# Optimization experiments

Hardware: AMD Instinct MI355X
Metric: run time of the kernel (lower is better)

## Reference

```python
import jax, jax.numpy as jnp
import numpy as np

# TT-matrix embedding: vocab = 50*60*60 = 180000, embed_dim = 8*8*8 = 512, tt_rank = 16
M1, M2, M3 = 50, 60, 60        # row modes (index factorization)
N1, N2, N3 = 8, 8, 8           # col modes (embedding-dim factorization)
R = 16                         # TT rank
SENT, BATCH = 2048, 64
VOCAB = M1 * M2 * M3


def setup_inputs() -> dict:
    key = jax.random.key(0)
    k1, k2, k3, kx = jax.random.split(key, 4)
    scale = 0.3  # per-core stddev (t3.random_matrix uses a similar per-core normal init)
    # core k stored with the gathered (row-mode) axis first so gather is a plain take
    core1 = jax.random.normal(k1, (M1, N1, R), dtype=jnp.float32) * scale       # [m1, n1, r]
    core2 = jax.random.normal(k2, (M2, R, N2, R), dtype=jnp.float32) * scale    # [m2, r, n2, r]
    core3 = jax.random.normal(k3, (M3, R, N3), dtype=jnp.float32) * scale       # [m3, r, n3]
    x = jax.random.randint(kx, (SENT, BATCH), 0, VOCAB, dtype=jnp.int64)        # batch_dim_last=True layout
    return {"x": x, "core1": core1, "core2": core2, "core3": core3}


def reference(x, core1, core2, core3):
    # batch_dim_last=True: x is [sent, batch] -> permute to [batch, sent]
    sent, batch = x.shape
    flat = x.T.reshape(-1)                      # [T] flat token ids, T = batch*sent
    # t3.ind2sub: row-major mixed-radix decomposition over row modes [M1, M2, M3]
    i1 = flat // (M2 * M3)
    rem = flat % (M2 * M3)
    i2 = rem // M3
    i3 = rem % M3
    # gather one slice per TT core
    g1 = core1[i1]                              # [T, n1, r]
    g2 = core2[i2]                              # [T, r, n2, r]
    g3 = core3[i3]                              # [T, r, n3]
    # contract cores -> full embedding rows (t3.gather_rows(...).full())
    t12 = jnp.einsum('tar,trbs->tabs', g1, g2)  # [T, n1, n2, r]
    emb = jnp.einsum('tabs,tsc->tabc', t12, g3) # [T, n1, n2, n3]
    rows = emb.reshape(batch, sent, N1 * N2 * N3)
    # batch_dim_last=True: permute back to [sent, batch, emb_dim]
    return rows.transpose(1, 0, 2)
```

## Files before the change

### kernel.cpp

```cpp
#include <hip/hip_runtime.h>
#include <hip/hip_bf16.h>


#define M2M3 3600u
#define M3 60u

__global__ __launch_bounds__(256) void tt_pair_kernel(
    const float* __restrict__ c1,
    const float* __restrict__ c2,
    float* __restrict__ tab)
{
    const int pair = blockIdx.x;
    const int i1 = pair / 60;
    const int i2 = pair - i1 * 60;
    const int tid = threadIdx.x;
    const int q  = tid >> 6;
    const int ab = tid & 63;
    const int a  = ab >> 3;
    const int b  = ab & 7;

    const float* __restrict__ g1 = c1 + i1 * 128 + a * 16;
    const float* __restrict__ g2 = c2 + i2 * 2048 + b * 16 + q * 4;

    float4 acc = make_float4(0.f, 0.f, 0.f, 0.f);
#pragma unroll
    for (int r = 0; r < 16; ++r) {
        const float a1 = g1[r];
        const float4 v = *(const float4*)(g2 + r * 128);
        acc.x = fmaf(a1, v.x, acc.x);
        acc.y = fmaf(a1, v.y, acc.y);
        acc.z = fmaf(a1, v.z, acc.z);
        acc.w = fmaf(a1, v.w, acc.w);
    }
    *(float4*)(tab + (size_t)pair * 1024 + tid * 4) = acc;
}

__global__ __launch_bounds__(256) void tt_embed2_kernel(
    const int* __restrict__ x,
    const float* __restrict__ c3,
    const float* __restrict__ tab,
    float* __restrict__ out,
    int T)
{
    const int u    = (int)((blockIdx.x * blockDim.x + threadIdx.x) >> 6);
    const int lane = threadIdx.x & 63;
    if (u >= T) return;

    const unsigned id  = __builtin_amdgcn_readfirstlane((unsigned)x[u]);
    const unsigned i1  = id / M2M3;
    const unsigned rem = id - i1 * M2M3;
    const unsigned i2  = rem / M3;
    const unsigned i3  = rem - i2 * M3;

    const float* tp = tab + (size_t)(i1 * 60u + i2) * 1024u;
    float4 t[4];
#pragma unroll
    for (int q = 0; q < 4; ++q)
        t[q] = *(const float4*)(tp + q * 256 + lane * 4);
    const float* tf = (const float*)t;

    const float4* __restrict__ g3 = (const float4*)(c3 + i3 * 128u);

    float o[8];
#pragma unroll
    for (int c = 0; c < 8; ++c) o[c] = 0.f;

#pragma unroll
    for (int s = 0; s < 16; ++s) {
        const float ts = tf[s];
        const float4 w0 = g3[s * 2 + 0];
        const float4 w1 = g3[s * 2 + 1];
        o[0] = fmaf(ts, w0.x, o[0]);
        o[1] = fmaf(ts, w0.y, o[1]);
        o[2] = fmaf(ts, w0.z, o[2]);
        o[3] = fmaf(ts, w0.w, o[3]);
        o[4] = fmaf(ts, w1.x, o[4]);
        o[5] = fmaf(ts, w1.y, o[5]);
        o[6] = fmaf(ts, w1.z, o[6]);
        o[7] = fmaf(ts, w1.w, o[7]);
    }

    float4* dst = (float4*)(out + (size_t)u * 512 + lane * 8);
    dst[0] = make_float4(o[0], o[1], o[2], o[3]);
    dst[1] = make_float4(o[4], o[5], o[6], o[7]);
}

__global__ __launch_bounds__(256) void tt_embed_kernel(
    const int* __restrict__ x, const float* __restrict__ c1,
    const float* __restrict__ c2, const float* __restrict__ c3,
    float* __restrict__ out, int T)
{
    const int u    = (int)((blockIdx.x * blockDim.x + threadIdx.x) >> 6);
    const int lane = threadIdx.x & 63;
    if (u >= T) return;
    const int a = lane >> 3, b = lane & 7;
    const unsigned id  = (unsigned)x[u];
    const unsigned i1  = id / M2M3;
    const unsigned rem = id - i1 * M2M3;
    const unsigned i2  = rem / M3;
    const unsigned i3  = rem - i2 * M3;
    const float4* g1 = (const float4*)(c1 + i1 * 128u + a * 16);
    const float*  g2 = c2 + i2 * 2048u + b * 16;
    const float4* g3 = (const float4*)(c3 + i3 * 128u);
    float4 a1v[4];
#pragma unroll
    for (int q = 0; q < 4; ++q) a1v[q] = g1[q];
    const float* a1f = (const float*)a1v;
    float t12[16];
#pragma unroll
    for (int s = 0; s < 16; ++s) t12[s] = 0.f;
#pragma unroll
    for (int r = 0; r < 16; ++r) {
        const float a1 = a1f[r];
        const float4* row = (const float4*)(g2 + r * 128);
#pragma unroll
        for (int q = 0; q < 4; ++q) {
            const float4 v = row[q];
            t12[q*4+0] = fmaf(a1, v.x, t12[q*4+0]);
            t12[q*4+1] = fmaf(a1, v.y, t12[q*4+1]);
            t12[q*4+2] = fmaf(a1, v.z, t12[q*4+2]);
            t12[q*4+3] = fmaf(a1, v.w, t12[q*4+3]);
        }
    }
    float o[8];
#pragma unroll
    for (int c = 0; c < 8; ++c) o[c] = 0.f;
#pragma unroll
    for (int s = 0; s < 16; ++s) {
        const float ts = t12[s];
        const float4 w0 = g3[s*2+0];
        const float4 w1 = g3[s*2+1];
        o[0]=fmaf(ts,w0.x,o[0]); o[1]=fmaf(ts,w0.y,o[1]);
        o[2]=fmaf(ts,w0.z,o[2]); o[3]=fmaf(ts,w0.w,o[3]);
        o[4]=fmaf(ts,w1.x,o[4]); o[5]=fmaf(ts,w1.y,o[5]);
        o[6]=fmaf(ts,w1.z,o[6]); o[7]=fmaf(ts,w1.w,o[7]);
    }
    float4* dst = (float4*)(out + (size_t)u * 512 + lane * 8);
    dst[0] = make_float4(o[0], o[1], o[2], o[3]);
    dst[1] = make_float4(o[4], o[5], o[6], o[7]);
}

extern "C" void kernel_launch(void* const* d_in, const int* in_sizes, int n_in,
                              void* d_out, int out_size, void* d_ws, size_t ws_size,
                              hipStream_t stream) {
    const int*   x  = (const int*)d_in[0];
    const float* c1 = (const float*)d_in[1];
    const float* c2 = (const float*)d_in[2];
    const float* c3 = (const float*)d_in[3];
    float* out = (float*)d_out;

    const int T = in_sizes[0];
    const size_t tab_bytes = 3000u * 1024u * sizeof(float);

    if (ws_size >= tab_bytes) {
        float* tab = (float*)d_ws;
        tt_pair_kernel<<<3000, 256, 0, stream>>>(c1, c2, tab);
        const int blocks = (T + 3) / 4;
        tt_embed2_kernel<<<blocks, 256, 0, stream>>>(x, c3, tab, out, T);
    } else {
        const int blocks = (T + 3) / 4;
        tt_embed_kernel<<<blocks, 256, 0, stream>>>(x, c1, c2, c3, out, T);
    }
}
```

Measured before the change: 334.3 us.

## Counting-sort tokens by (i1,i2) pair to reuse precomputed table rows

Adds a counting sort of tokens by their (i1,i2) pair index (histogram, single-block scan, atomic scatter) so each wavefront handles a chunk of tokens sharing table rows and reloads the 4KB pair row only when the pair changes. This is meant to cut redundant gathers from the 12MB pair table. It adds four extra kernel launches, global atomics, and scattered output writes, since consecutive sorted tokens land at random output rows.

```diff
diff --git a/kernel.cpp b/kernel.cpp
--- a/kernel.cpp
+++ b/kernel.cpp
@@ -1,9 +1,10 @@
 #include <hip/hip_runtime.h>
-#include <hip/hip_bf16.h>
 
 
 #define M2M3 3600u
-#define M3 60u
+#define M3   60u
+#define NPAIR 3000
+#define CHUNK 16
 
 __global__ __launch_bounds__(256) void tt_pair_kernel(
     const float* __restrict__ c1,
@@ -35,51 +36,156 @@
     *(float4*)(tab + (size_t)pair * 1024 + tid * 4) = acc;
 }
 
-__global__ __launch_bounds__(256) void tt_embed2_kernel(
-    const int* __restrict__ x,
+__global__ __launch_bounds__(256) void tt_zero_counts(unsigned* __restrict__ counts)
+{
+    const int i = blockIdx.x * blockDim.x + threadIdx.x;
+    if (i < NPAIR) counts[i] = 0u;
+}
+
+__global__ __launch_bounds__(256) void tt_hist(
+    const int* __restrict__ x, unsigned* __restrict__ counts, int T)
+{
+    const int t = blockIdx.x * blockDim.x + threadIdx.x;
+    if (t >= T) return;
+    const unsigned id = (unsigned)x[t];
+    atomicAdd(&counts[id / M3], 1u);
+}
+
+__global__ __launch_bounds__(1024) void tt_scan(
+    const unsigned* __restrict__ counts, unsigned* __restrict__ cursor)
+{
+    __shared__ unsigned buf[1024];
+    const int tid = threadIdx.x;
+    const int b = tid * 3;
+    unsigned c0 = 0, c1 = 0, c2 = 0;
+    if (b     < NPAIR) c0 = counts[b];
+    if (b + 1 < NPAIR) c1 = counts[b + 1];
+    if (b + 2 < NPAIR) c2 = counts[b + 2];
+    const unsigned local = c0 + c1 + c2;
+    buf[tid] = local;
+    __syncthreads();
+    for (int off = 1; off < 1024; off <<= 1) {
+        const unsigned v = (tid >= off) ? buf[tid - off] : 0u;
+        __syncthreads();
+        buf[tid] += v;
+        __syncthreads();
+    }
+    const unsigned excl = buf[tid] - local;
+    if (b     < NPAIR) cursor[b]     = excl;
+    if (b + 1 < NPAIR) cursor[b + 1] = excl + c0;
+    if (b + 2 < NPAIR) cursor[b + 2] = excl + c0 + c1;
+}
+
+__global__ __launch_bounds__(256) void tt_scatter(
+    const int* __restrict__ x, unsigned* __restrict__ cursor,
+    unsigned* __restrict__ recT, unsigned* __restrict__ recPI, int T)
+{
+    const int t = blockIdx.x * blockDim.x + threadIdx.x;
+    if (t >= T) return;
+    const unsigned id   = (unsigned)x[t];
+    const unsigned pair = id / M3;
+    const unsigned i3   = id - pair * M3;
+    const unsigned pos  = atomicAdd(&cursor[pair], 1u);
+    recT[pos]  = (unsigned)t;
+    recPI[pos] = (pair << 6) | i3;
+}
+
+__global__ __launch_bounds__(256) void tt_embed_sorted(
+    const unsigned* __restrict__ recT,
+    const unsigned* __restrict__ recPI,
     const float* __restrict__ c3,
     const float* __restrict__ tab,
     float* __restrict__ out,
     int T)
 {
+    const int wid  = (int)((blockIdx.x * blockDim.x + threadIdx.x) >> 6);
+    const int lane = threadIdx.x & 63;
+    const int base = wid * CHUNK;
+    if (base >= T) return;
+
+    unsigned rT = 0u, rP = 0u;
+    if (lane < CHUNK && base + lane < T) {
+        rT = recT[base + lane];
+        rP = recPI[base + lane];
+    }
+
+    const int n = min(CHUNK, T - base);
+    float4 t4[4];
+    int cur = -1;
+
+    for (int j = 0; j < n; ++j) {
+        const unsigned tt = __builtin_amdgcn_readlane(rT, j);
+        const unsigned pi = __builtin_amdgcn_readlane(rP, j);
+        const int      pair = (int)(pi >> 6);
+        const unsigned i3   = pi & 63u;
+
+        if (pair != cur) {
+            cur = pair;
+            const float* tp = tab + (size_t)pair * 1024u;
+#pragma unroll
+            for (int q = 0; q < 4; ++q)
+                t4[q] = *(const float4*)(tp + q * 256 + lane * 4);
+        }
+        const float* tf = (const float*)t4;
+
+        const float4* __restrict__ g3 = (const float4*)(c3 + i3 * 128u);
+
+        float o[8];
+#pragma unroll
+        for (int c = 0; c < 8; ++c) o[c] = 0.f;
+#pragma unroll
+        for (int s = 0; s < 16; ++s) {
+            const float ts = tf[s];
+            const float4 w0 = g3[s * 2 + 0];
+            const float4 w1 = g3[s * 2 + 1];
+            o[0] = fmaf(ts, w0.x, o[0]);
+            o[1] = fmaf(ts, w0.y, o[1]);
+            o[2] = fmaf(ts, w0.z, o[2]);
+            o[3] = fmaf(ts, w0.w, o[3]);
+            o[4] = fmaf(ts, w1.x, o[4]);
+            o[5] = fmaf(ts, w1.y, o[5]);
+            o[6] = fmaf(ts, w1.z, o[6]);
+            o[7] = fmaf(ts, w1.w, o[7]);
+        }
+
+        float4* dst = (float4*)(out + (size_t)tt * 512u + lane * 8);
+        dst[0] = make_float4(o[0], o[1], o[2], o[3]);
+        dst[1] = make_float4(o[4], o[5], o[6], o[7]);
+    }
+}
+
+__global__ __launch_bounds__(256) void tt_embed2_kernel(
+    const int* __restrict__ x, const float* __restrict__ c3,
+    const float* __restrict__ tab, float* __restrict__ out, int T)
+{
     const int u    = (int)((blockIdx.x * blockDim.x + threadIdx.x) >> 6);
     const int lane = threadIdx.x & 63;
     if (u >= T) return;
-
     const unsigned id  = __builtin_amdgcn_readfirstlane((unsigned)x[u]);
     const unsigned i1  = id / M2M3;
     const unsigned rem = id - i1 * M2M3;
     const unsigned i2  = rem / M3;
     const unsigned i3  = rem - i2 * M3;
-
     const float* tp = tab + (size_t)(i1 * 60u + i2) * 1024u;
     float4 t[4];
 #pragma unroll
     for (int q = 0; q < 4; ++q)
         t[q] = *(const float4*)(tp + q * 256 + lane * 4);
     const float* tf = (const float*)t;
-
     const float4* __restrict__ g3 = (const float4*)(c3 + i3 * 128u);
-
     float o[8];
 #pragma unroll
     for (int c = 0; c < 8; ++c) o[c] = 0.f;
-
 #pragma unroll
     for (int s = 0; s < 16; ++s) {
         const float ts = tf[s];
         const float4 w0 = g3[s * 2 + 0];
         const float4 w1 = g3[s * 2 + 1];
-        o[0] = fmaf(ts, w0.x, o[0]);
-        o[1] = fmaf(ts, w0.y, o[1]);
-        o[2] = fmaf(ts, w0.z, o[2]);
-        o[3] = fmaf(ts, w0.w, o[3]);
-        o[4] = fmaf(ts, w1.x, o[4]);
-        o[5] = fmaf(ts, w1.y, o[5]);
-        o[6] = fmaf(ts, w1.z, o[6]);
-        o[7] = fmaf(ts, w1.w, o[7]);
-    }
-
+        o[0]=fmaf(ts,w0.x,o[0]); o[1]=fmaf(ts,w0.y,o[1]);
+        o[2]=fmaf(ts,w0.z,o[2]); o[3]=fmaf(ts,w0.w,o[3]);
+        o[4]=fmaf(ts,w1.x,o[4]); o[5]=fmaf(ts,w1.y,o[5]);
+        o[6]=fmaf(ts,w1.z,o[6]); o[7]=fmaf(ts,w1.w,o[7]);
+    }
     float4* dst = (float4*)(out + (size_t)u * 512 + lane * 8);
     dst[0] = make_float4(o[0], o[1], o[2], o[3]);
     dst[1] = make_float4(o[4], o[5], o[6], o[7]);
@@ -150,11 +256,34 @@
     float* out = (float*)d_out;
 
     const int T = in_sizes[0];
-    const size_t tab_bytes = 3000u * 1024u * sizeof(float);
-
-    if (ws_size >= tab_bytes) {
-        float* tab = (float*)d_ws;
-        tt_pair_kernel<<<3000, 256, 0, stream>>>(c1, c2, tab);
+
+    const size_t tab_bytes  = (size_t)NPAIR * 1024u * sizeof(float);
+    const size_t off_counts = tab_bytes;
+    const size_t off_cursor = off_counts + 12032;
+    const size_t off_recT   = off_cursor + 12032;
+    const size_t off_recPI  = off_recT + (size_t)T * 4u;
+    const size_t need_sort  = off_recPI + (size_t)T * 4u;
+
+    char* ws = (char*)d_ws;
+
+    if (ws_size >= need_sort) {
+        float*    tab    = (float*)ws;
+        unsigned* counts = (unsigned*)(ws + off_counts);
+        unsigned* cursor = (unsigned*)(ws + off_cursor);
+        unsigned* recT   = (unsigned*)(ws + off_recT);
+        unsigned* recPI  = (unsigned*)(ws + off_recPI);
+
+        tt_pair_kernel<<<NPAIR, 256, 0, stream>>>(c1, c2, tab);
+        tt_zero_counts<<<(NPAIR + 255) / 256, 256, 0, stream>>>(counts);
+        tt_hist<<<(T + 255) / 256, 256, 0, stream>>>(x, counts, T);
+        tt_scan<<<1, 1024, 0, stream>>>(counts, cursor);
+        tt_scatter<<<(T + 255) / 256, 256, 0, stream>>>(x, cursor, recT, recPI, T);
+        const int waves  = (T + CHUNK - 1) / CHUNK;
+        const int blocks = (waves + 3) / 4;
+        tt_embed_sorted<<<blocks, 256, 0, stream>>>(recT, recPI, c3, tab, out, T);
+    } else if (ws_size >= tab_bytes) {
+        float* tab = (float*)ws;
+        tt_pair_kernel<<<NPAIR, 256, 0, stream>>>(c1, c2, tab);
         const int blocks = (T + 3) / 4;
         tt_embed2_kernel<<<blocks, 256, 0, stream>>>(x, c3, tab, out, T);
     } else {
```

Result: no change. 328.3 us (-1.8%).
